# Performance work log

Hardware: AMD Instinct MI355X
Metric: run time of the kernel (lower is better)

The kernel has to match this reference:

```python
import jax, jax.numpy as jnp
import numpy as np
from jax import lax

VOCAB = 100   # chars_count
E = 32        # CHARACTER_EMBEDDING_SIZE
H = 64        # CHAR_LSTM_HIDDEN_SIZE
N_WORDS = 65536
MAX_LEN = 16


def setup_inputs() -> dict:
    key = jax.random.key(0)
    k_ch, k_len, k_emb, k_wih, k_whh, k_bih, k_bhh = jax.random.split(key, 7)
    chars = jax.random.randint(k_ch, (N_WORDS, MAX_LEN), 0, VOCAB, dtype=jnp.int32)
    lengths = jax.random.randint(k_len, (N_WORDS,), 1, MAX_LEN + 1, dtype=jnp.int32)
    s = 1.0 / np.sqrt(H)  # torch LSTM default init scale
    emb = jax.random.normal(k_emb, (VOCAB, E), dtype=jnp.float32)
    W_ih = jax.random.uniform(k_wih, (4 * H, E), minval=-s, maxval=s, dtype=jnp.float32)
    W_hh = jax.random.uniform(k_whh, (4 * H, H), minval=-s, maxval=s, dtype=jnp.float32)
    b_ih = jax.random.uniform(k_bih, (4 * H,), minval=-s, maxval=s, dtype=jnp.float32)
    b_hh = jax.random.uniform(k_bhh, (4 * H,), minval=-s, maxval=s, dtype=jnp.float32)
    return {"emb": emb, "W_ih": W_ih, "W_hh": W_hh, "b_ih": b_ih, "b_hh": b_hh,
            "chars": chars, "lengths": lengths}


def _char_lstm(emb, W_ih, W_hh, b_ih, b_hh, chars, lengths):
    N, L = chars.shape
    h0 = jnp.zeros((N, H), dtype=emb.dtype)
    c0 = jnp.zeros((N, H), dtype=emb.dtype)

    def step(carry, inp):
        h, c = carry
        ch_t, t = inp  # ch_t: [N] char ids at timestep t
        x = emb[ch_t]  # [N, E]
        gates = x @ W_ih.T + b_ih + h @ W_hh.T + b_hh  # [N, 4H]
        i_g, f_g, g_g, o_g = jnp.split(gates, 4, axis=-1)  # torch order i,f,g,o
        i_g = jax.nn.sigmoid(i_g)
        f_g = jax.nn.sigmoid(f_g)
        g_g = jnp.tanh(g_g)
        o_g = jax.nn.sigmoid(o_g)
        c_new = f_g * c + i_g * g_g
        h_new = o_g * jnp.tanh(c_new)
        active = (t < lengths)[:, None]  # freeze state past word end -> out[-1]
        h = jnp.where(active, h_new, h)
        c = jnp.where(active, c_new, c)
        return (h, c), None

    (h_final, _), _ = lax.scan(step, (h0, c0), (chars.T, jnp.arange(L)))
    return h_final  # [N, H] = last valid hidden per word


def reference(emb, W_ih, W_hh, b_ih, b_hh, chars, lengths):
    return _char_lstm(emb, W_ih, W_hh, b_ih, b_hh, chars, lengths)
```

## Files before the change

kernel.cpp:

```cpp
#include <hip/hip_runtime.h>
#include <hip/hip_bf16.h>


#define VOCAB 100
#define E     32
#define NH    64
#define NW    65536
#define MAXL  16
#define NGRP  4096

typedef __bf16 bf16x8 __attribute__((ext_vector_type(8)));
typedef float  f32x4  __attribute__((ext_vector_type(4)));
typedef unsigned short ushort_t;
typedef unsigned int uint_t;

__device__ __forceinline__ ushort_t f2bf(float x) {
    union { __hip_bfloat16 b; ushort_t u; } cv;
    cv.b = __float2bfloat16(x);
    return cv.u;
}
__device__ __forceinline__ float sigm(float x) {
    return __fdividef(1.f, 1.f + __expf(-x));
}
__device__ __forceinline__ float tanh_(float x) {
    return 1.f - __fdividef(2.f, __expf(2.f * x) + 1.f);
}

__global__ void prep_fused(const float* __restrict__ emb, const float* __restrict__ Wih,
                           const float* __restrict__ Whh, const float* __restrict__ bih,
                           const float* __restrict__ bhh, const int* __restrict__ lengths,
                           float* __restrict__ xtab, ushort_t* __restrict__ Wb,
                           int* __restrict__ bh) {
    int bid = blockIdx.x;
    if (bid < VOCAB) {
        int ch = bid, g = threadIdx.x;
        float acc = bih[g] + bhh[g];
        const float* er = emb + ch * E;
        const float* wr = Wih + g * E;
        #pragma unroll
        for (int e = 0; e < E; ++e) acc = fmaf(er[e], wr[e], acc);
        xtab[ch * 256 + g] = acc;
    } else if (bid < VOCAB + 64) {
        int i = (bid - VOCAB) * 256 + threadIdx.x;
        Wb[i] = f2bf(Whh[i]);
    } else {
        int blk = bid - (VOCAB + 64);
        __shared__ int h[16];
        if (threadIdx.x < 16) h[threadIdx.x] = 0;
        __syncthreads();
        atomicAdd(&h[lengths[blk * 256 + threadIdx.x] - 1], 1);
        __syncthreads();
        if (threadIdx.x < 16) bh[blk * 16 + threadIdx.x] = h[threadIdx.x];
    }
}

__global__ void k_bases(const int* __restrict__ bh, int* __restrict__ bases) {
    __shared__ int tot[16], bb[16];
    int b = threadIdx.x;
    if (b < 16) { int s = 0; for (int blk = 0; blk < 256; ++blk) s += bh[blk * 16 + b]; tot[b] = s; }
    __syncthreads();
    if (threadIdx.x == 0) { int a = 0; for (int i = 0; i < 16; ++i) { bb[i] = a; a += tot[i]; } }
    __syncthreads();
    if (b < 16) { int a = bb[b]; for (int blk = 0; blk < 256; ++blk) { bases[blk * 16 + b] = a; a += bh[blk * 16 + b]; } }
}

__global__ void k_scatter(const int* __restrict__ lengths, const int* __restrict__ bases,
                          int* __restrict__ perm) {
    __shared__ int h[16];
    if (threadIdx.x < 16) h[threadIdx.x] = 0;
    __syncthreads();
    int w = blockIdx.x * 256 + threadIdx.x;
    int b = lengths[w] - 1;
    int r = atomicAdd(&h[b], 1);
    perm[bases[blockIdx.x * 16 + b] + r] = w;
}

__global__ __launch_bounds__(256, 2) void lstm_main(
    const ushort_t* __restrict__ Wb, const float* __restrict__ xtab,
    const int* __restrict__ chars, const int* __restrict__ lengths,
    const int* __restrict__ perm, float* __restrict__ out)
{
    __shared__ __align__(16) char Hlds_all[4][2048];
    char* Hbase = Hlds_all[threadIdx.x >> 6];

    const int lane = threadIdx.x & 63;
    const int w  = lane & 15;
    const int lq = lane >> 4;
    const int wave = (blockIdx.x << 2) + (threadIdx.x >> 6);

    bf16x8 a[16][2];
    #pragma unroll
    for (int m = 0; m < 16; ++m)
        #pragma unroll
        for (int kh = 0; kh < 2; ++kh)
            a[m][kh] = *reinterpret_cast<const bf16x8*>(Wb + ((m * 16 + w) * 64 + kh * 32 + lq * 8));

    const int sw = (w & 7) << 4;
    const int base_w = w * 128;
    int wr_off[4], rd_off[2];
    #pragma unroll
    for (int b = 0; b < 4; ++b) wr_off[b] = base_w + ((b * 32 + lq * 8) ^ sw);
    #pragma unroll
    for (int kh = 0; kh < 2; ++kh) rd_off[kh] = base_w + ((kh * 64 + lq * 16) ^ sw);

    #pragma unroll 1
    for (int gi = 0; gi < 2; ++gi) {
        const int grp = gi ? (NGRP - 1 - wave) : wave;
        const int wid = perm[grp * 16 + w];
        const int len = lengths[wid];
        const int maxl = __builtin_amdgcn_readlane(len, 15);
        const int* chp = chars + wid * MAXL;

        float hreg[4][4], creg[4][4];
        #pragma unroll
        for (int b = 0; b < 4; ++b)
            #pragma unroll
            for (int r = 0; r < 4; ++r) { hreg[b][r] = 0.f; creg[b][r] = 0.f; }

        int ch = chp[0];
        const float* xrow = xtab + ch * 256;
        f32x4 xtb[2][4];
        #pragma unroll
        for (int q = 0; q < 4; ++q)
            xtb[0][q] = *reinterpret_cast<const f32x4*>(xrow + (q * 4 + 0) * 16 + lq * 4);

        #pragma unroll 1
        for (int t = 0; t < maxl; ++t) {
            const int tn = (t + 1 < maxl) ? t + 1 : t;
            const int ch_nxt = chp[tn];
            const float* xrow_n = xtab + ch_nxt * 256;

            bf16x8 B0, B1;
            if (t > 0) {
                asm volatile("s_waitcnt lgkmcnt(0)" ::: "memory");
                B0 = *reinterpret_cast<const bf16x8*>(Hbase + rd_off[0]);
                B1 = *reinterpret_cast<const bf16x8*>(Hbase + rd_off[1]);
            }
            const bool act = (t < len);

            #pragma unroll
            for (int b = 0; b < 4; ++b) {
                if (b < 3) {
                    #pragma unroll
                    for (int q = 0; q < 4; ++q)
                        xtb[(b + 1) & 1][q] = *reinterpret_cast<const f32x4*>(xrow + (q * 4 + b + 1) * 16 + lq * 4);
                } else {
                    #pragma unroll
                    for (int q = 0; q < 4; ++q)
                        xtb[0][q] = *reinterpret_cast<const f32x4*>(xrow_n + q * 64 + lq * 4);
                }
                f32x4 d[4];
                #pragma unroll
                for (int q = 0; q < 4; ++q) d[q] = xtb[b & 1][q];
                if (t > 0) {
                    #pragma unroll
                    for (int q = 0; q < 4; ++q) {
                        d[q] = __builtin_amdgcn_mfma_f32_16x16x32_bf16(a[q * 4 + b][0], B0, d[q], 0, 0, 0);
                        d[q] = __builtin_amdgcn_mfma_f32_16x16x32_bf16(a[q * 4 + b][1], B1, d[q], 0, 0, 0);
                    }
                }
                #pragma unroll
                for (int r = 0; r < 4; ++r) {
                    float ig = sigm(d[0][r]);
                    float fg = sigm(d[1][r]);
                    float gg = tanh_(d[2][r]);
                    float og = sigm(d[3][r]);
                    float cn = fmaf(fg, creg[b][r], ig * gg);
                    float hn = og * tanh_(cn);
                    creg[b][r] = act ? cn : creg[b][r];
                    hreg[b][r] = act ? hn : hreg[b][r];
                }
                uint_t lo = (uint_t)f2bf(hreg[b][0]) | ((uint_t)f2bf(hreg[b][1]) << 16);
                uint_t hi = (uint_t)f2bf(hreg[b][2]) | ((uint_t)f2bf(hreg[b][3]) << 16);
                *reinterpret_cast<uint2*>(Hbase + wr_off[b]) = make_uint2(lo, hi);
            }
            ch = ch_nxt;
            xrow = xrow_n;
        }

        #pragma unroll
        for (int b = 0; b < 4; ++b) {
            f32x4 o;
            #pragma unroll
            for (int r = 0; r < 4; ++r) o[r] = hreg[b][r];
            *reinterpret_cast<f32x4*>(out + wid * 64 + b * 16 + lq * 4) = o;
        }
    }
}

extern "C" void kernel_launch(void* const* d_in, const int* in_sizes, int n_in,
                              void* d_out, int out_size, void* d_ws, size_t ws_size,
                              hipStream_t stream) {
    const float* emb = (const float*)d_in[0];
    const float* Wih = (const float*)d_in[1];
    const float* Whh = (const float*)d_in[2];
    const float* bih = (const float*)d_in[3];
    const float* bhh = (const float*)d_in[4];
    const int* chars = (const int*)d_in[5];
    const int* lens  = (const int*)d_in[6];
    float* out = (float*)d_out;

    float*    xtab = (float*)d_ws;
    ushort_t* Wb   = (ushort_t*)(xtab + 25600);
    int*      bh   = (int*)(Wb + 16384);
    int*      bas  = bh + 4096;
    int*      perm = bas + 4096;

    prep_fused<<<VOCAB + 64 + 256, 256, 0, stream>>>(emb, Wih, Whh, bih, bhh, lens, xtab, Wb, bh);
    k_bases<<<1, 64, 0, stream>>>(bh, bas);
    k_scatter<<<256, 256, 0, stream>>>(lens, bas, perm);

    lstm_main<<<512, 256, 0, stream>>>(Wb, xtab, chars, lens, perm, out);
}
```

Baseline: 192.5 us.

## Fold exp2 scaling into weights, parallelize prefix scan, one group per wave

```diff
diff --git a/kernel.cpp b/kernel.cpp
--- a/kernel.cpp
+++ b/kernel.cpp
@@ -4,7 +4,6 @@
 
 #define VOCAB 100
 #define E     32
-#define NH    64
 #define NW    65536
 #define MAXL  16
 #define NGRP  4096
@@ -14,17 +13,16 @@
 typedef unsigned short ushort_t;
 typedef unsigned int uint_t;
 
+#define LOG2E    1.4426950408889634f
+#define TWOLOG2E 2.8853900817779268f
+
 __device__ __forceinline__ ushort_t f2bf(float x) {
     union { __hip_bfloat16 b; ushort_t u; } cv;
     cv.b = __float2bfloat16(x);
     return cv.u;
 }
-__device__ __forceinline__ float sigm(float x) {
-    return __fdividef(1.f, 1.f + __expf(-x));
-}
-__device__ __forceinline__ float tanh_(float x) {
-    return 1.f - __fdividef(2.f, __expf(2.f * x) + 1.f);
-}
+__device__ __forceinline__ float exp2_hw(float x) { return __builtin_amdgcn_exp2f(x); }
+__device__ __forceinline__ float rcp_hw(float x)  { return __builtin_amdgcn_rcpf(x); }
 
 __global__ void prep_fused(const float* __restrict__ emb, const float* __restrict__ Wih,
                            const float* __restrict__ Whh, const float* __restrict__ bih,
@@ -33,16 +31,19 @@
                            int* __restrict__ bh) {
     int bid = blockIdx.x;
     if (bid < VOCAB) {
-        int ch = bid, g = threadIdx.x;
+        int ch = bid, g = threadIdx.x, q = g >> 6;
+        float scl = (q == 2) ? TWOLOG2E : -LOG2E;
         float acc = bih[g] + bhh[g];
         const float* er = emb + ch * E;
         const float* wr = Wih + g * E;
         #pragma unroll
         for (int e = 0; e < E; ++e) acc = fmaf(er[e], wr[e], acc);
-        xtab[ch * 256 + g] = acc;
+        xtab[ch * 256 + g] = acc * scl;
     } else if (bid < VOCAB + 64) {
         int i = (bid - VOCAB) * 256 + threadIdx.x;
-        Wb[i] = f2bf(Whh[i]);
+        int q = i >> 12;
+        float scl = (q == 2) ? TWOLOG2E : -LOG2E;
+        Wb[i] = f2bf(Whh[i] * scl);
     } else {
         int blk = bid - (VOCAB + 64);
         __shared__ int h[16];
@@ -55,13 +56,26 @@
 }
 
 __global__ void k_bases(const int* __restrict__ bh, int* __restrict__ bases) {
-    __shared__ int tot[16], bb[16];
-    int b = threadIdx.x;
-    if (b < 16) { int s = 0; for (int blk = 0; blk < 256; ++blk) s += bh[blk * 16 + b]; tot[b] = s; }
-    __syncthreads();
-    if (threadIdx.x == 0) { int a = 0; for (int i = 0; i < 16; ++i) { bb[i] = a; a += tot[i]; } }
-    __syncthreads();
-    if (b < 16) { int a = bb[b]; for (int blk = 0; blk < 256; ++blk) { bases[blk * 16 + b] = a; a += bh[blk * 16 + b]; } }
+    __shared__ int chunk[16][16], chunkpre[16][16], tot[16], gb[16];
+    int t = threadIdx.x, b = t & 15, cs = t >> 4;
+    int s = 0;
+    #pragma unroll
+    for (int i = 0; i < 16; ++i) s += bh[(cs * 16 + i) * 16 + b];
+    chunk[cs][b] = s;
+    __syncthreads();
+    if (t < 16) {
+        int a = 0;
+        for (int c2 = 0; c2 < 16; ++c2) { chunkpre[c2][b] = a; a += chunk[c2][b]; }
+        tot[b] = a;
+    }
+    __syncthreads();
+    if (t == 0) { int a = 0; for (int i = 0; i < 16; ++i) { gb[i] = a; a += tot[i]; } }
+    __syncthreads();
+    int base = gb[b] + chunkpre[cs][b];
+    for (int i = 0; i < 16; ++i) {
+        bases[(cs * 16 + i) * 16 + b] = base;
+        base += bh[(cs * 16 + i) * 16 + b];
+    }
 }
 
 __global__ void k_scatter(const int* __restrict__ lengths, const int* __restrict__ bases,
@@ -75,7 +89,7 @@
     perm[bases[blockIdx.x * 16 + b] + r] = w;
 }
 
-__global__ __launch_bounds__(256, 2) void lstm_main(
+__global__ __launch_bounds__(256, 4) void lstm_main(
     const ushort_t* __restrict__ Wb, const float* __restrict__ xtab,
     const int* __restrict__ chars, const int* __restrict__ lengths,
     const int* __restrict__ perm, float* __restrict__ out)
@@ -86,7 +100,9 @@
     const int lane = threadIdx.x & 63;
     const int w  = lane & 15;
     const int lq = lane >> 4;
-    const int wave = (blockIdx.x << 2) + (threadIdx.x >> 6);
+    const int widx = threadIdx.x >> 6;
+    const int cls  = ((blockIdx.x & 3) << 2) | widx;
+    const int grp  = (cls << 8) | (blockIdx.x >> 2);
 
     bf16x8 a[16][2];
     #pragma unroll
@@ -103,88 +119,90 @@
     #pragma unroll
     for (int kh = 0; kh < 2; ++kh) rd_off[kh] = base_w + ((kh * 64 + lq * 16) ^ sw);
 
+    const int wid = perm[grp * 16 + w];
+    const int len = lengths[wid];
+    int ml = len;
+    ml = max(ml, __shfl_xor(ml, 1));
+    ml = max(ml, __shfl_xor(ml, 2));
+    ml = max(ml, __shfl_xor(ml, 4));
+    ml = max(ml, __shfl_xor(ml, 8));
+    const int maxl = __builtin_amdgcn_readfirstlane(ml);
+    const int* chp = chars + wid * MAXL;
+
+    float hreg[4][4], creg[4][4];
+    #pragma unroll
+    for (int b = 0; b < 4; ++b)
+        #pragma unroll
+        for (int r = 0; r < 4; ++r) { hreg[b][r] = 0.f; creg[b][r] = 0.f; }
+
+    int ch = chp[0];
+    const float* xrow = xtab + ch * 256;
+    f32x4 xtb[2][4];
+    #pragma unroll
+    for (int q = 0; q < 4; ++q)
+        xtb[0][q] = *reinterpret_cast<const f32x4*>(xrow + (q * 4 + 0) * 16 + lq * 4);
+
     #pragma unroll 1
-    for (int gi = 0; gi < 2; ++gi) {
-        const int grp = gi ? (NGRP - 1 - wave) : wave;
-        const int wid = perm[grp * 16 + w];
-        const int len = lengths[wid];
-        const int maxl = __builtin_amdgcn_readlane(len, 15);
-        const int* chp = chars + wid * MAXL;
-
-        float hreg[4][4], creg[4][4];
-        #pragma unroll
-        for (int b = 0; b < 4; ++b)
+    for (int t = 0; t < maxl; ++t) {
+        const int tn = (t + 1 < maxl) ? t + 1 : t;
+        const int ch_nxt = chp[tn];
+        const float* xrow_n = xtab + ch_nxt * 256;
+
+        bf16x8 B0, B1;
+        if (t > 0) {
+            asm volatile("s_waitcnt lgkmcnt(0)" ::: "memory");
+            B0 = *reinterpret_cast<const bf16x8*>(Hbase + rd_off[0]);
+            B1 = *reinterpret_cast<const bf16x8*>(Hbase + rd_off[1]);
+        }
+        const bool act = (t < len);
+
+        #pragma unroll
+        for (int b = 0; b < 4; ++b) {
+            if (b < 3) {
+                #pragma unroll
+                for (int q = 0; q < 4; ++q)
+                    xtb[(b + 1) & 1][q] = *reinterpret_cast<const f32x4*>(xrow + (q * 4 + b + 1) * 16 + lq * 4);
+            } else {
+                #pragma unroll
+                for (int q = 0; q < 4; ++q)
+                    xtb[0][q] = *reinterpret_cast<const f32x4*>(xrow_n + q * 64 + lq * 4);
+            }
+            f32x4 d[4];
             #pragma unroll
-            for (int r = 0; r < 4; ++r) { hreg[b][r] = 0.f; creg[b][r] = 0.f; }
-
-        int ch = chp[0];
-        const float* xrow = xtab + ch * 256;
-        f32x4 xtb[2][4];
-        #pragma unroll
-        for (int q = 0; q < 4; ++q)
-            xtb[0][q] = *reinterpret_cast<const f32x4*>(xrow + (q * 4 + 0) * 16 + lq * 4);
-
-        #pragma unroll 1
-        for (int t = 0; t < maxl; ++t) {
-            const int tn = (t + 1 < maxl) ? t + 1 : t;
-            const int ch_nxt = chp[tn];
-            const float* xrow_n = xtab + ch_nxt * 256;
-
-            bf16x8 B0, B1;
+            for (int q = 0; q < 4; ++q) d[q] = xtb[b & 1][q];
             if (t > 0) {
-                asm volatile("s_waitcnt lgkmcnt(0)" ::: "memory");
-                B0 = *reinterpret_cast<const bf16x8*>(Hbase + rd_off[0]);
-                B1 = *reinterpret_cast<const bf16x8*>(Hbase + rd_off[1]);
+                #pragma unroll
+                for (int q = 0; q < 4; ++q) {
+                    d[q] = __builtin_amdgcn_mfma_f32_16x16x32_bf16(a[q * 4 + b][0], B0, d[q], 0, 0, 0);
+                    d[q] = __builtin_amdgcn_mfma_f32_16x16x32_bf16(a[q * 4 + b][1], B1, d[q], 0, 0, 0);
+                }
             }
-            const bool act = (t < len);
-
             #pragma unroll
-            for (int b = 0; b < 4; ++b) {
-                if (b < 3) {
-                    #pragma unroll
-                    for (int q = 0; q < 4; ++q)
-                        xtb[(b + 1) & 1][q] = *reinterpret_cast<const f32x4*>(xrow + (q * 4 + b + 1) * 16 + lq * 4);
-                } else {
-                    #pragma unroll
-                    for (int q = 0; q < 4; ++q)
-                        xtb[0][q] = *reinterpret_cast<const f32x4*>(xrow_n + q * 64 + lq * 4);
-                }
-                f32x4 d[4];
-                #pragma unroll
-                for (int q = 0; q < 4; ++q) d[q] = xtb[b & 1][q];
-                if (t > 0) {
-                    #pragma unroll
-                    for (int q = 0; q < 4; ++q) {
-                        d[q] = __builtin_amdgcn_mfma_f32_16x16x32_bf16(a[q * 4 + b][0], B0, d[q], 0, 0, 0);
-                        d[q] = __builtin_amdgcn_mfma_f32_16x16x32_bf16(a[q * 4 + b][1], B1, d[q], 0, 0, 0);
-                    }
-                }
-                #pragma unroll
-                for (int r = 0; r < 4; ++r) {
-                    float ig = sigm(d[0][r]);
-                    float fg = sigm(d[1][r]);
-                    float gg = tanh_(d[2][r]);
-                    float og = sigm(d[3][r]);
-                    float cn = fmaf(fg, creg[b][r], ig * gg);
-                    float hn = og * tanh_(cn);
-                    creg[b][r] = act ? cn : creg[b][r];
-                    hreg[b][r] = act ? hn : hreg[b][r];
-                }
-                uint_t lo = (uint_t)f2bf(hreg[b][0]) | ((uint_t)f2bf(hreg[b][1]) << 16);
-                uint_t hi = (uint_t)f2bf(hreg[b][2]) | ((uint_t)f2bf(hreg[b][3]) << 16);
-                *reinterpret_cast<uint2*>(Hbase + wr_off[b]) = make_uint2(lo, hi);
+            for (int r = 0; r < 4; ++r) {
+                float ig = rcp_hw(1.f + exp2_hw(d[0][r]));
+                float fg = rcp_hw(1.f + exp2_hw(d[1][r]));
+                float gg = fmaf(-2.f, rcp_hw(1.f + exp2_hw(d[2][r])), 1.f);
+                float og = rcp_hw(1.f + exp2_hw(d[3][r]));
+                float cn = fmaf(fg, creg[b][r], ig * gg);
+                float tc = fmaf(-2.f, rcp_hw(1.f + exp2_hw(cn * TWOLOG2E)), 1.f);
+                float hn = og * tc;
+                creg[b][r] = act ? cn : creg[b][r];
+                hreg[b][r] = act ? hn : hreg[b][r];
             }
-            ch = ch_nxt;
-            xrow = xrow_n;
+            uint_t lo = (uint_t)f2bf(hreg[b][0]) | ((uint_t)f2bf(hreg[b][1]) << 16);
+            uint_t hi = (uint_t)f2bf(hreg[b][2]) | ((uint_t)f2bf(hreg[b][3]) << 16);
+            *reinterpret_cast<uint2*>(Hbase + wr_off[b]) = make_uint2(lo, hi);
         }
-
-        #pragma unroll
-        for (int b = 0; b < 4; ++b) {
-            f32x4 o;
-            #pragma unroll
-            for (int r = 0; r < 4; ++r) o[r] = hreg[b][r];
-            *reinterpret_cast<f32x4*>(out + wid * 64 + b * 16 + lq * 4) = o;
-        }
+        ch = ch_nxt;
+        xrow = xrow_n;
+    }
+
+    #pragma unroll
+    for (int b = 0; b < 4; ++b) {
+        f32x4 o;
+        #pragma unroll
+        for (int r = 0; r < 4; ++r) o[r] = hreg[b][r];
+        *reinterpret_cast<f32x4*>(out + wid * 64 + b * 16 + lq * 4) = o;
     }
 }
 
@@ -207,8 +225,8 @@
     int*      perm = bas + 4096;
 
     prep_fused<<<VOCAB + 64 + 256, 256, 0, stream>>>(emb, Wih, Whh, bih, bhh, lens, xtab, Wb, bh);
-    k_bases<<<1, 64, 0, stream>>>(bh, bas);
+    k_bases<<<1, 256, 0, stream>>>(bh, bas);
     k_scatter<<<256, 256, 0, stream>>>(lens, bas, perm);
 
-    lstm_main<<<512, 256, 0, stream>>>(Wb, xtab, chars, lens, perm, out);
-}
+    lstm_main<<<1024, 256, 0, stream>>>(Wb, xtab, chars, lens, perm, out);
+}
```

New measurement: 346.4 us. +79.9%, slower.
